# Optimization experiments

Measured on AMD Instinct MI355X. Metric: run time of the kernel, lower is better.

Reference implementation:

```python
import jax, jax.numpy as jnp
import numpy as np

B, S, NE, E, H = 4, 2048, 8, 1024, 16
DH = E // H


def setup_inputs() -> dict:
    key = jax.random.key(0)
    ks = jax.random.split(key, 10)
    s = 0.02
    return {
        "x": jax.random.normal(ks[0], (B, S, E), dtype=jnp.float32),
        "w1": jax.random.normal(ks[1], (NE, 4 * E, E), dtype=jnp.float32) * s,
        "b1": jnp.zeros((NE, 4 * E), dtype=jnp.float32),
        "w2": jax.random.normal(ks[2], (NE, E, 4 * E), dtype=jnp.float32) * s,
        "b2": jnp.zeros((NE, E), dtype=jnp.float32),
        "in_proj_w": jax.random.normal(ks[3], (3 * E, E), dtype=jnp.float32) * s,
        "in_proj_b": jnp.zeros((3 * E,), dtype=jnp.float32),
        "out_w": jax.random.normal(ks[4], (E, E), dtype=jnp.float32) * s,
        "out_b": jnp.zeros((E,), dtype=jnp.float32),
        "expert_id": 3,
    }


def reference(x, w1, b1, w2, b2, in_proj_w, in_proj_b, out_w, out_b, expert_id):
    # Per-expert FFN: [B,S,E] -> [B,S,NE,E]
    h = jax.nn.relu(jnp.einsum("bse,nfe->bsnf", x, w1) + b1)
    eo = jnp.einsum("bsnf,nef->bsne", h, w2) + b2  # [B,S,NE,E]

    # Multihead self-attention over the expert axis, batched over (B,S).
    wq, wk, wv = in_proj_w[:E], in_proj_w[E:2 * E], in_proj_w[2 * E:]
    bq, bk, bv = in_proj_b[:E], in_proj_b[E:2 * E], in_proj_b[2 * E:]
    q = (eo @ wq.T + bq).reshape(B, S, NE, H, DH)
    k = (eo @ wk.T + bk).reshape(B, S, NE, H, DH)
    v = (eo @ wv.T + bv).reshape(B, S, NE, H, DH)

    scale = 1.0 / jnp.sqrt(jnp.asarray(DH, dtype=q.dtype))
    # torch additive float mask: tril of ONES added to logits (not -inf masking)
    add_mask = jnp.tril(jnp.ones((NE, NE), dtype=q.dtype))
    logits = jnp.einsum("bsqhd,bskhd->bshqk", q, k) * scale + add_mask
    attn = jax.nn.softmax(logits, axis=-1)
    o = jnp.einsum("bshqk,bskhd->bsqhd", attn, v).reshape(B, S, NE, E)
    o = o @ out_w.T + out_b  # [B,S,NE,E]

    return o[:, :, expert_id, :]  # [B,S,E]
```

## Files before the change

### kernel.cpp

```cpp
#include <hip/hip_runtime.h>

typedef __bf16 bf16x8 __attribute__((ext_vector_type(8)));
typedef float  f32x4  __attribute__((ext_vector_type(4)));

__device__ __forceinline__ float bf2f(unsigned short u) {
    union { unsigned int i; float f; } x; x.i = ((unsigned int)u) << 16; return x.f;
}
__device__ __forceinline__ unsigned short f2bf(float f) {
    union { float f; unsigned int i; } x; x.f = f;
    unsigned int r = x.i + 0x7fff + ((x.i >> 16) & 1);
    return (unsigned short)(r >> 16);
}

__device__ __forceinline__ void gload16(const void* g, void* l) {
    __builtin_amdgcn_global_load_lds(
        (const __attribute__((address_space(1))) void*)g,
        (__attribute__((address_space(3))) void*)l, 16, 0, 0);
}

__global__ __launch_bounds__(256) void cvt_f32_bf16(
    const float4* __restrict__ in, ushort4* __restrict__ out, long n4)
{
    long i = (long)blockIdx.x * blockDim.x + threadIdx.x;
    const long stride = (long)gridDim.x * blockDim.x;
    for (; i < n4; i += stride) {
        const float4 v = in[i];
        ushort4 o = { f2bf(v.x), f2bf(v.y), f2bf(v.z), f2bf(v.w) };
        out[i] = o;
    }
}

template<bool RELU, typename CT>
__global__ __launch_bounds__(256, 4) void gemm_nt(
    const ushort* __restrict__ A, long lda, long sAz,
    const ushort* __restrict__ B, long ldb, long sBz,
    const float* __restrict__ bias, long sBiasz,
    CT* __restrict__ C, long ldc, long sCz,
    int K, const int* __restrict__ eid_p, int eidSel)
{
    const long z = eidSel ? (long)(*eid_p) : (long)blockIdx.z;
    A    += z * sAz;
    B    += z * sBz;
    bias += z * sBiasz;
    C    += z * sCz;

    __shared__ alignas(16) ushort As[128 * 32];
    __shared__ alignas(16) ushort Bs[128 * 32];

    const int t    = threadIdx.x;
    const int w    = t >> 6;
    const int lane = t & 63;
    const int lr   = lane & 15;
    const int lq   = lane >> 4;
    const int wm   = (w >> 1) * 64;
    const int wn   = (w & 1) * 64;
    const long m0  = (long)blockIdx.y * 128;
    const long n0  = (long)blockIdx.x * 128;

    const int srow   = t >> 2;
    const int schunk = (t & 3) * 8;
    const ushort* aG = A + (m0 + srow) * lda + schunk;
    const ushort* bG = B + (n0 + srow) * ldb + schunk;
    char* lA = (char*)As + w * 1024;
    char* lB = (char*)Bs + w * 1024;

    f32x4 acc[4][4];
#pragma unroll
    for (int i = 0; i < 4; i++)
#pragma unroll
        for (int j = 0; j < 4; j++) acc[i][j] = (f32x4){0.f, 0.f, 0.f, 0.f};

    for (int kt = 0; kt < K; kt += 32) {
        gload16(aG,            lA);
        gload16(aG + 64 * lda, lA + 4096);
        gload16(bG,            lB);
        gload16(bG + 64 * ldb, lB + 4096);
        aG += 32; bG += 32;
        __syncthreads();

        bf16x8 af[4], bf[4];
#pragma unroll
        for (int i = 0; i < 4; i++)
            af[i] = *(const bf16x8*)&As[(wm + i * 16 + lr) * 32 + lq * 8];
#pragma unroll
        for (int j = 0; j < 4; j++)
            bf[j] = *(const bf16x8*)&Bs[(wn + j * 16 + lr) * 32 + lq * 8];
#pragma unroll
        for (int i = 0; i < 4; i++)
#pragma unroll
            for (int j = 0; j < 4; j++)
                acc[i][j] = __builtin_amdgcn_mfma_f32_16x16x32_bf16(af[i], bf[j], acc[i][j], 0, 0, 0);
        __syncthreads();
    }

#pragma unroll
    for (int j = 0; j < 4; j++) {
        const long col = n0 + wn + j * 16 + lr;
        const float bv = bias[col];
#pragma unroll
        for (int i = 0; i < 4; i++) {
            const long rbase = m0 + wm + i * 16 + lq * 4;
#pragma unroll
            for (int r = 0; r < 4; r++) {
                float v = acc[i][j][r] + bv;
                if (RELU) v = fmaxf(v, 0.f);
                if constexpr (__is_same(CT, ushort)) C[(rbase + r) * ldc + col] = f2bf(v);
                else                                 C[(rbase + r) * ldc + col] = v;
            }
        }
    }
}

__global__ __launch_bounds__(256) void attn_kernel(
    const ushort* __restrict__ q, const ushort* __restrict__ kv,
    const int* __restrict__ eid_p, ushort* __restrict__ o3)
{
    const size_t m = blockIdx.x;
    const int t    = threadIdx.x;
    const int h    = t >> 4;
    const int d0   = (t & 15) * 4;
    const int eid  = *eid_p;

    const ushort4 qu = *(const ushort4*)(q + m * 1024 + h * 64 + d0);
    const float qv[4] = { bf2f(qu.x), bf2f(qu.y), bf2f(qu.z), bf2f(qu.w) };

    float l[8];
#pragma unroll
    for (int n = 0; n < 8; n++) {
        const ushort4 ku = *(const ushort4*)(kv + (m * 8 + n) * 2048 + h * 64 + d0);
        float p = qv[0] * bf2f(ku.x) + qv[1] * bf2f(ku.y) + qv[2] * bf2f(ku.z) + qv[3] * bf2f(ku.w);
        p += __shfl_xor(p, 1);
        p += __shfl_xor(p, 2);
        p += __shfl_xor(p, 4);
        p += __shfl_xor(p, 8);
        l[n] = p * 0.125f + ((n <= eid) ? 1.0f : 0.0f);
    }
    float mx = l[0];
#pragma unroll
    for (int n = 1; n < 8; n++) mx = fmaxf(mx, l[n]);
    float e[8], s = 0.f;
#pragma unroll
    for (int n = 0; n < 8; n++) { e[n] = __expf(l[n] - mx); s += e[n]; }
    const float inv = 1.f / s;

    float o[4] = {0.f, 0.f, 0.f, 0.f};
#pragma unroll
    for (int n = 0; n < 8; n++) {
        const ushort4 vu = *(const ushort4*)(kv + (m * 8 + n) * 2048 + 1024 + h * 64 + d0);
        const float a = e[n] * inv;
        o[0] += a * bf2f(vu.x); o[1] += a * bf2f(vu.y);
        o[2] += a * bf2f(vu.z); o[3] += a * bf2f(vu.w);
    }
    ushort4 ou = { f2bf(o[0]), f2bf(o[1]), f2bf(o[2]), f2bf(o[3]) };
    *(ushort4*)(o3 + m * 1024 + h * 64 + d0) = ou;
}

extern "C" void kernel_launch(void* const* d_in, const int* in_sizes, int n_in,
                              void* d_out, int out_size, void* d_ws, size_t ws_size,
                              hipStream_t stream)
{
    const float* x   = (const float*)d_in[0];
    const float* w1  = (const float*)d_in[1];
    const float* b1  = (const float*)d_in[2];
    const float* w2  = (const float*)d_in[3];
    const float* b2  = (const float*)d_in[4];
    const float* ipw = (const float*)d_in[5];
    const float* ipb = (const float*)d_in[6];
    const float* ow  = (const float*)d_in[7];
    const float* ob  = (const float*)d_in[8];
    const int*   eid = (const int*)d_in[9];

    char* ws = (char*)d_ws;
    size_t off = 0;
    auto alloc = [&](size_t bytes) { char* p = ws + off; off += (bytes + 255) & ~(size_t)255; return p; };
    ushort* w1b  = (ushort*)alloc(8LL * 4096 * 1024 * 2);
    ushort* w2b  = (ushort*)alloc(8LL * 1024 * 4096 * 2);
    ushort* ipwb = (ushort*)alloc(3LL * 1024 * 1024 * 2);
    ushort* owb  = (ushort*)alloc(1LL * 1024 * 1024 * 2);
    ushort* xb   = (ushort*)alloc(8192LL * 1024 * 2);
    ushort* kvb  = (ushort*)alloc(8192LL * 8 * 2048 * 2);
    ushort* qb   = (ushort*)alloc(8192LL * 1024 * 2);
    const size_t fixed = off;

    long Mc = 8192;
    while (Mc > 256 && fixed + (size_t)Mc * 81920 + 1024 > ws_size) Mc >>= 1;
    ushort* hb  = (ushort*)alloc((size_t)Mc * 8 * 4096 * 2);
    ushort* eob = (ushort*)alloc((size_t)Mc * 8 * 1024 * 2);
    ushort* o3b = hb;

    const dim3 blk(256);
    const dim3 cgrid(2048);

    cvt_f32_bf16<<<cgrid, blk, 0, stream>>>((const float4*)w1,  (ushort4*)w1b,  8LL * 4096 * 1024 / 4);
    cvt_f32_bf16<<<cgrid, blk, 0, stream>>>((const float4*)w2,  (ushort4*)w2b,  8LL * 1024 * 4096 / 4);
    cvt_f32_bf16<<<cgrid, blk, 0, stream>>>((const float4*)ipw, (ushort4*)ipwb, 3LL * 1024 * 1024 / 4);
    cvt_f32_bf16<<<cgrid, blk, 0, stream>>>((const float4*)ow,  (ushort4*)owb,  1LL * 1024 * 1024 / 4);
    cvt_f32_bf16<<<cgrid, blk, 0, stream>>>((const float4*)x,   (ushort4*)xb,   8192LL * 1024 / 4);

    for (long m0 = 0; m0 < 8192; m0 += Mc) {
        const unsigned my = (unsigned)(Mc / 128);
        gemm_nt<true, ushort><<<dim3(32, my, 8), blk, 0, stream>>>(
            xb + m0 * 1024, 1024, 0,
            w1b, 1024, 4096LL * 1024,
            b1, 4096,
            hb, 4096, (long)Mc * 4096,
            1024, eid, 0);
        gemm_nt<false, ushort><<<dim3(8, my, 8), blk, 0, stream>>>(
            hb, 4096, (long)Mc * 4096,
            w2b, 4096, 1024LL * 4096,
            b2, 1024,
            eob, 1024, (long)Mc * 1024,
            4096, eid, 0);
        gemm_nt<false, ushort><<<dim3(16, my, 8), blk, 0, stream>>>(
            eob, 1024, (long)Mc * 1024,
            ipwb + (size_t)1024 * 1024, 1024, 0,
            ipb + 1024, 0,
            kvb + m0 * 16384, 16384, 2048,
            1024, eid, 0);
        gemm_nt<false, ushort><<<dim3(8, my, 1), blk, 0, stream>>>(
            eob, 1024, (long)Mc * 1024,
            ipwb, 1024, 0,
            ipb, 0,
            qb + m0 * 1024, 1024, 0,
            1024, eid, 1);
    }

    attn_kernel<<<dim3(8192), blk, 0, stream>>>(qb, kvb, eid, o3b);

    gemm_nt<false, float><<<dim3(8, 64, 1), blk, 0, stream>>>(
        o3b, 1024, 0,
        owb, 1024, 0,
        ob, 0,
        (float*)d_out, 1024, 0,
        1024, eid, 0);
}
```

Before: 2.666 ms.

## Fuse Q and KV projections into one GEMM and chunk attention per slice

Q and KV projections now run in a single gemm_qkv launch over 24 column tiles. Blocks covering Q columns exit early unless their z matches the expert id. The attention kernel moves inside the M-chunk loop and reads chunk-sized Q/KV buffers, and the chunk size is capped at 2048 rows. The aim is fewer launches and a much smaller KV working set that may stay in cache. The trade-off is more launches per chunk, smaller grids, and idle blocks in the fused GEMM.

```diff
diff --git a/kernel.cpp b/kernel.cpp
--- a/kernel.cpp
+++ b/kernel.cpp
@@ -30,15 +30,16 @@
     }
 }
 
+
 template<bool RELU, typename CT>
 __global__ __launch_bounds__(256, 4) void gemm_nt(
     const ushort* __restrict__ A, long lda, long sAz,
     const ushort* __restrict__ B, long ldb, long sBz,
     const float* __restrict__ bias, long sBiasz,
     CT* __restrict__ C, long ldc, long sCz,
-    int K, const int* __restrict__ eid_p, int eidSel)
-{
-    const long z = eidSel ? (long)(*eid_p) : (long)blockIdx.z;
+    int K)
+{
+    const long z = blockIdx.z;
     A    += z * sAz;
     B    += z * sBz;
     bias += z * sBiasz;
@@ -111,8 +112,88 @@
     }
 }
 
+__global__ __launch_bounds__(256, 4) void gemm_qkv(
+    const ushort* __restrict__ A, long lda, long sAz,
+    const ushort* __restrict__ B, long ldb,
+    const float* __restrict__ bias,
+    ushort* __restrict__ qc,
+    ushort* __restrict__ kvc,
+    int K, const int* __restrict__ eid_p)
+{
+    const long z   = blockIdx.z;
+    const long n0  = (long)blockIdx.x * 128;
+    const bool isq = (n0 < 1024);
+    if (isq && z != (long)(*eid_p)) return;
+    A += z * sAz;
+
+    __shared__ alignas(16) ushort As[128 * 32];
+    __shared__ alignas(16) ushort Bs[128 * 32];
+
+    const int t    = threadIdx.x;
+    const int w    = t >> 6;
+    const int lane = t & 63;
+    const int lr   = lane & 15;
+    const int lq   = lane >> 4;
+    const int wm   = (w >> 1) * 64;
+    const int wn   = (w & 1) * 64;
+    const long m0  = (long)blockIdx.y * 128;
+
+    const int srow   = t >> 2;
+    const int schunk = (t & 3) * 8;
+    const ushort* aG = A + (m0 + srow) * lda + schunk;
+    const ushort* bG = B + (n0 + srow) * ldb + schunk;
+    char* lA = (char*)As + w * 1024;
+    char* lB = (char*)Bs + w * 1024;
+
+    f32x4 acc[4][4];
+#pragma unroll
+    for (int i = 0; i < 4; i++)
+#pragma unroll
+        for (int j = 0; j < 4; j++) acc[i][j] = (f32x4){0.f, 0.f, 0.f, 0.f};
+
+    for (int kt = 0; kt < K; kt += 32) {
+        gload16(aG,            lA);
+        gload16(aG + 64 * lda, lA + 4096);
+        gload16(bG,            lB);
+        gload16(bG + 64 * ldb, lB + 4096);
+        aG += 32; bG += 32;
+        __syncthreads();
+
+        bf16x8 af[4], bf[4];
+#pragma unroll
+        for (int i = 0; i < 4; i++)
+            af[i] = *(const bf16x8*)&As[(wm + i * 16 + lr) * 32 + lq * 8];
+#pragma unroll
+        for (int j = 0; j < 4; j++)
+            bf[j] = *(const bf16x8*)&Bs[(wn + j * 16 + lr) * 32 + lq * 8];
+#pragma unroll
+        for (int i = 0; i < 4; i++)
+#pragma unroll
+            for (int j = 0; j < 4; j++)
+                acc[i][j] = __builtin_amdgcn_mfma_f32_16x16x32_bf16(af[i], bf[j], acc[i][j], 0, 0, 0);
+        __syncthreads();
+    }
+
+#pragma unroll
+    for (int j = 0; j < 4; j++) {
+        const long col = n0 + wn + j * 16 + lr;
+        const float bv = bias[col];
+#pragma unroll
+        for (int i = 0; i < 4; i++) {
+            const long rbase = m0 + wm + i * 16 + lq * 4;
+#pragma unroll
+            for (int r = 0; r < 4; r++) {
+                const float v = acc[i][j][r] + bv;
+                const long row = rbase + r;
+                if (isq) qc[row * 1024 + col] = f2bf(v);
+                else     kvc[row * 16384 + z * 2048 + (col - 1024)] = f2bf(v);
+            }
+        }
+    }
+}
+
 __global__ __launch_bounds__(256) void attn_kernel(
-    const ushort* __restrict__ q, const ushort* __restrict__ kv,
+    const ushort* __restrict__ qc, const ushort* __restrict__ kvc,
     const int* __restrict__ eid_p, ushort* __restrict__ o3)
 {
     const size_t m = blockIdx.x;
@@ -121,13 +202,13 @@
     const int d0   = (t & 15) * 4;
     const int eid  = *eid_p;
 
-    const ushort4 qu = *(const ushort4*)(q + m * 1024 + h * 64 + d0);
+    const ushort4 qu = *(const ushort4*)(qc + m * 1024 + h * 64 + d0);
     const float qv[4] = { bf2f(qu.x), bf2f(qu.y), bf2f(qu.z), bf2f(qu.w) };
 
     float l[8];
 #pragma unroll
     for (int n = 0; n < 8; n++) {
-        const ushort4 ku = *(const ushort4*)(kv + (m * 8 + n) * 2048 + h * 64 + d0);
+        const ushort4 ku = *(const ushort4*)(kvc + (m * 8 + n) * 2048 + h * 64 + d0);
         float p = qv[0] * bf2f(ku.x) + qv[1] * bf2f(ku.y) + qv[2] * bf2f(ku.z) + qv[3] * bf2f(ku.w);
         p += __shfl_xor(p, 1);
         p += __shfl_xor(p, 2);
@@ -146,7 +227,7 @@
     float o[4] = {0.f, 0.f, 0.f, 0.f};
 #pragma unroll
     for (int n = 0; n < 8; n++) {
-        const ushort4 vu = *(const ushort4*)(kv + (m * 8 + n) * 2048 + 1024 + h * 64 + d0);
+        const ushort4 vu = *(const ushort4*)(kvc + (m * 8 + n) * 2048 + 1024 + h * 64 + d0);
         const float a = e[n] * inv;
         o[0] += a * bf2f(vu.x); o[1] += a * bf2f(vu.y);
         o[2] += a * bf2f(vu.z); o[3] += a * bf2f(vu.w);
@@ -178,15 +259,15 @@
     ushort* ipwb = (ushort*)alloc(3LL * 1024 * 1024 * 2);
     ushort* owb  = (ushort*)alloc(1LL * 1024 * 1024 * 2);
     ushort* xb   = (ushort*)alloc(8192LL * 1024 * 2);
-    ushort* kvb  = (ushort*)alloc(8192LL * 8 * 2048 * 2);
-    ushort* qb   = (ushort*)alloc(8192LL * 1024 * 2);
+    ushort* o3b  = (ushort*)alloc(8192LL * 1024 * 2);
     const size_t fixed = off;
 
-    long Mc = 8192;
-    while (Mc > 256 && fixed + (size_t)Mc * 81920 + 1024 > ws_size) Mc >>= 1;
+    long Mc = 2048;
+    while (Mc > 256 && fixed + (size_t)Mc * 116736 + 2048 > ws_size) Mc >>= 1;
     ushort* hb  = (ushort*)alloc((size_t)Mc * 8 * 4096 * 2);
     ushort* eob = (ushort*)alloc((size_t)Mc * 8 * 1024 * 2);
-    ushort* o3b = hb;
+    ushort* kvc = (ushort*)alloc((size_t)Mc * 8 * 2048 * 2);
+    ushort* qc  = (ushort*)alloc((size_t)Mc * 1024 * 2);
 
     const dim3 blk(256);
     const dim3 cgrid(2048);
@@ -204,33 +285,27 @@
             w1b, 1024, 4096LL * 1024,
             b1, 4096,
             hb, 4096, (long)Mc * 4096,
-            1024, eid, 0);
+            1024);
         gemm_nt<false, ushort><<<dim3(8, my, 8), blk, 0, stream>>>(
             hb, 4096, (long)Mc * 4096,
             w2b, 4096, 1024LL * 4096,
             b2, 1024,
             eob, 1024, (long)Mc * 1024,
-            4096, eid, 0);
-        gemm_nt<false, ushort><<<dim3(16, my, 8), blk, 0, stream>>>(
+            4096);
+        gemm_qkv<<<dim3(24, my, 8), blk, 0, stream>>>(
             eob, 1024, (long)Mc * 1024,
-            ipwb + (size_t)1024 * 1024, 1024, 0,
-            ipb + 1024, 0,
-            kvb + m0 * 16384, 16384, 2048,
-            1024, eid, 0);
-        gemm_nt<false, ushort><<<dim3(8, my, 1), blk, 0, stream>>>(
-            eob, 1024, (long)Mc * 1024,
-            ipwb, 1024, 0,
-            ipb, 0,
-            qb + m0 * 1024, 1024, 0,
-            1024, eid, 1);
-    }
-
-    attn_kernel<<<dim3(8192), blk, 0, stream>>>(qb, kvb, eid, o3b);
+            ipwb, 1024,
+            ipb,
+            qc, kvc,
+            1024, eid);
+        attn_kernel<<<dim3((unsigned)Mc), blk, 0, stream>>>(
+            qc, kvc, eid, o3b + m0 * 1024);
+    }
 
     gemm_nt<false, float><<<dim3(8, 64, 1), blk, 0, stream>>>(
         o3b, 1024, 0,
         owb, 1024, 0,
         ob, 0,
         (float*)d_out, 1024, 0,
-        1024, eid, 0);
-}
+        1024);
+}
```

Result: faster. 2.461 ms (-7.7%).
